# Kernel optimization log

Hardware: AMD Instinct MI355X
Metric: run time of the kernel (lower is better)

## Reference

```python
import jax, jax.numpy as jnp
import numpy as np

B, IN, H = 8192, 1024, 1024

def setup_inputs() -> dict:
    key = jax.random.key(0)
    ks = jax.random.split(key, 12)
    s_i = 1.0 / np.sqrt(IN)   # lecun-normal-ish scale for input kernels
    s_h = 1.0 / np.sqrt(H)
    d = {
        'inputs': jax.random.normal(ks[0], (B, IN), jnp.float32),
        'c': jax.random.normal(ks[1], (B, H), jnp.float32),
        'h': jax.random.normal(ks[2], (B, H), jnp.float32),
    }
    for n, k in zip(['Wii', 'Wif', 'Wig', 'Wio'], ks[3:7]):
        d[n] = jax.random.normal(k, (IN, H), jnp.float32) * s_i
    for n, k in zip(['Whi', 'Whf', 'Whg', 'Who'], ks[7:11]):
        d[n] = jax.random.normal(k, (H, H), jnp.float32) * s_h
    for n in ['bi', 'bf', 'bg', 'bo']:
        d[n] = jnp.zeros((H,), jnp.float32)
    return d

def reference(inputs, c, h, Wii, Wif, Wig, Wio, Whi, Whf, Whg, Who, bi, bf, bg, bo):
    # i = sigmoid(x Wii + h Whi + bi); f, o likewise; g = tanh(x Wig + h Whg + bg)
    i = jax.nn.sigmoid(inputs @ Wii + h @ Whi + bi)
    f = jax.nn.sigmoid(inputs @ Wif + h @ Whf + bf)
    g = jnp.tanh(inputs @ Wig + h @ Whg + bg)
    o = jax.nn.sigmoid(inputs @ Wio + h @ Who + bo)
    new_c = f * c + i * g
    new_h = o * jnp.tanh(new_c)
    return (new_c, new_h)
```

## Files before the change

kernel.cpp:

```cpp
#include <hip/hip_runtime.h>
#include <hip/hip_bf16.h>
#include <cstdint>


#define B_DIM 8192
#define H_DIM 1024
#define K2    2048
#define N4    4096
#define BK    64
#define BM    256
#define BN    256
#define NT    (K2 / BK)

typedef __bf16 bf16x8 __attribute__((ext_vector_type(8)));
typedef float  f32x4  __attribute__((ext_vector_type(4)));

__device__ __forceinline__ void async_load16(const __bf16* g, __bf16* l) {
  __builtin_amdgcn_global_load_lds(
      (__attribute__((address_space(1))) void*)(g),
      (__attribute__((address_space(3))) void*)(l),
      16, 0, 0);
}

__device__ __forceinline__ float sigm(float x) {
  return 1.0f / (1.0f + __expf(-x));
}
__device__ __forceinline__ float tanh_fast(float x) {
  return 2.0f / (1.0f + __expf(-2.0f * x)) - 1.0f;
}

__global__ void cast_a(const float* __restrict__ x, const float* __restrict__ h,
                       __bf16* __restrict__ A) {
  int row = blockIdx.x;
  int k = threadIdx.x << 3;
  const float* src = (k < H_DIM) ? (x + (size_t)row * H_DIM + k)
                                 : (h + (size_t)row * H_DIM + (k - H_DIM));
  float4 v0 = *(const float4*)src;
  float4 v1 = *(const float4*)(src + 4);
  bf16x8 o;
  o[0] = (__bf16)v0.x; o[1] = (__bf16)v0.y; o[2] = (__bf16)v0.z; o[3] = (__bf16)v0.w;
  o[4] = (__bf16)v1.x; o[5] = (__bf16)v1.y; o[6] = (__bf16)v1.z; o[7] = (__bf16)v1.w;
  *(bf16x8*)&A[(size_t)row * K2 + k] = o;
}

__global__ void cast_w(const float* __restrict__ Wii, const float* __restrict__ Wif,
                       const float* __restrict__ Wig, const float* __restrict__ Wio,
                       const float* __restrict__ Whi, const float* __restrict__ Whf,
                       const float* __restrict__ Whg, const float* __restrict__ Who,
                       __bf16* __restrict__ Bt) {
  __shared__ float tile[64][33];
  int k0 = blockIdx.x * 64;
  int j0 = blockIdx.y * 32;
  int gate = blockIdx.z;
  const float* Wi[4] = {Wii, Wif, Wig, Wio};
  const float* Wh[4] = {Whi, Whf, Whg, Who};
  const float* W = (k0 < H_DIM) ? Wi[gate] : Wh[gate];
  int kb = (k0 < H_DIM) ? k0 : (k0 - H_DIM);

  int col = threadIdx.x & 31;
  int rr  = threadIdx.x >> 5;
#pragma unroll
  for (int p = 0; p < 8; ++p)
    tile[p * 8 + rr][col] = W[(size_t)(kb + p * 8 + rr) * H_DIM + j0 + col];
  __syncthreads();

  int jj = threadIdx.x >> 3;
  int ko = threadIdx.x & 7;
  int j = j0 + jj;
  int p = ((j >> 4) << 6) + (gate << 4) + (j & 15);
  bf16x8 o;
#pragma unroll
  for (int t = 0; t < 8; ++t) o[t] = (__bf16)tile[ko * 8 + t][jj];
  *(bf16x8*)&Bt[(size_t)p * K2 + k0 + ko * 8] = o;
}


#define STAGE_A(D, KH, TT) do { \
    async_load16(gA0 + (size_t)(TT) * 64 + (KH) * 32, &As_s[D][KH][wave << 9]); \
    async_load16(gA1 + (size_t)(TT) * 64 + (KH) * 32, &As_s[D][KH][4096 + (wave << 9)]); \
  } while (0)
#define STAGE_B(D, KH, TT) do { \
    async_load16(gB0 + (size_t)(TT) * 64 + (KH) * 32, &Bs_s[D][KH][wave << 9]); \
    async_load16(gB1 + (size_t)(TT) * 64 + (KH) * 32, &Bs_s[D][KH][4096 + (wave << 9)]); \
  } while (0)

#define LOADA(D, KK, MH) do { \
    const __bf16* ap_ = &As_s[D][KK][(wm << 12) + ((MH) << 11) + lane_part]; \
    aF[0] = *(const bf16x8*)(ap_); \
    aF[1] = *(const bf16x8*)(ap_ + 512); \
    aF[2] = *(const bf16x8*)(ap_ + 1024); \
    aF[3] = *(const bf16x8*)(ap_ + 1536); \
  } while (0)
#define LOADB(D, KK) do { \
    const __bf16* bp_ = &Bs_s[D][KK][(wn << 11) + lane_part]; \
    bF[0] = *(const bf16x8*)(bp_); \
    bF[1] = *(const bf16x8*)(bp_ + 512); \
    bF[2] = *(const bf16x8*)(bp_ + 1024); \
    bF[3] = *(const bf16x8*)(bp_ + 1536); \
  } while (0)

#define BARW() do { \
    __builtin_amdgcn_s_barrier(); \
    asm volatile("s_waitcnt lgkmcnt(0)" ::: "memory"); \
    __builtin_amdgcn_sched_barrier(0); \
  } while (0)
#define ENDBAR() __builtin_amdgcn_s_barrier()
#define GATE8() asm volatile("s_waitcnt vmcnt(8)" ::: "memory")
#define GATE4() asm volatile("s_waitcnt vmcnt(4)" ::: "memory")
#define GATE0() asm volatile("s_waitcnt vmcnt(0)" ::: "memory")

#define MFMA_Q(MH) do { \
    __builtin_amdgcn_s_setprio(1); \
    _Pragma("unroll") \
    for (int i2 = 0; i2 < 4; ++i2) { \
      _Pragma("unroll") \
      for (int n2 = 0; n2 < 4; ++n2) \
        acc[(MH) * 4 + i2][n2] = __builtin_amdgcn_mfma_f32_16x16x32_bf16( \
            aF[i2], bF[n2], acc[(MH) * 4 + i2][n2], 0, 0, 0); \
    } \
    __builtin_amdgcn_s_setprio(0); \
  } while (0)

__global__ __launch_bounds__(512, 2) void lstm_gemm(
    const __bf16* __restrict__ A,
    const __bf16* __restrict__ Bt,
    const float* __restrict__ c,
    const float* __restrict__ bi, const float* __restrict__ bf_,
    const float* __restrict__ bg, const float* __restrict__ bo,
    float* __restrict__ out_c, float* __restrict__ out_h) {
  __shared__ __align__(16) __bf16 As_s[2][2][256 * 32];
  __shared__ __align__(16) __bf16 Bs_s[2][2][256 * 32];

  const int wg  = blockIdx.x;
  const int swz = ((wg & 7) << 6) + (wg >> 3);
  const int bx = swz & 31;
  const int by = swz >> 5;
  const int m0 = bx << 8;
  const int n0 = by << 8;

  const int tid  = threadIdx.x;
  const int wave = tid >> 6;
  const int lane = tid & 63;
  const int wm   = wave >> 2;
  const int wn   = wave & 3;

  const int srow = (wave << 4) + (lane >> 2);
  const int sgc  = (lane & 3) ^ ((lane >> 3) & 3);
  const __bf16* gA0 = A  + (size_t)(m0 + srow) * K2 + sgc * 8;
  const __bf16* gA1 = gA0 + (size_t)128 * K2;
  const __bf16* gB0 = Bt + (size_t)(n0 + srow) * K2 + sgc * 8;
  const __bf16* gB1 = gB0 + (size_t)128 * K2;

  const int lane_part = ((lane & 15) << 5) + ((((lane >> 4) ^ ((lane >> 1) & 3))) << 3);

  f32x4 acc[8][4] = {};
  bf16x8 aF[4], bF[4];

  STAGE_A(0, 0, 0); STAGE_B(0, 0, 0);
  STAGE_A(0, 1, 0); STAGE_B(0, 1, 0);
  STAGE_A(1, 0, 1); STAGE_B(1, 0, 1);
  GATE8();
  __builtin_amdgcn_s_barrier();

  for (int t = 0; t < NT - 2; ++t) {
    const int db = t & 1;
    LOADA(db, 0, 0); LOADB(db, 0); STAGE_A(db ^ 1, 1, t + 1);
    BARW(); MFMA_Q(0); ENDBAR();
    LOADA(db, 0, 1); STAGE_B(db ^ 1, 1, t + 1);
    BARW(); MFMA_Q(1); GATE8(); ENDBAR();
    LOADA(db, 1, 0); LOADB(db, 1); STAGE_A(db, 0, t + 2);
    BARW(); MFMA_Q(0); ENDBAR();
    LOADA(db, 1, 1); STAGE_B(db, 0, t + 2);
    BARW(); MFMA_Q(1); GATE8(); ENDBAR();
  }

  {
    LOADA(0, 0, 0); LOADB(0, 0); STAGE_A(1, 1, NT - 1);
    BARW(); MFMA_Q(0); ENDBAR();
    LOADA(0, 0, 1); STAGE_B(1, 1, NT - 1);
    BARW(); MFMA_Q(1); GATE8(); ENDBAR();
    LOADA(0, 1, 0); LOADB(0, 1);
    BARW(); MFMA_Q(0); ENDBAR();
    LOADA(0, 1, 1);
    BARW(); MFMA_Q(1); GATE4(); ENDBAR();
  }
  {
    LOADA(1, 0, 0); LOADB(1, 0);
    BARW(); MFMA_Q(0); ENDBAR();
    LOADA(1, 0, 1);
    BARW(); MFMA_Q(1); GATE0(); ENDBAR();
    LOADA(1, 1, 0); LOADB(1, 1);
    BARW(); MFMA_Q(0); ENDBAR();
    LOADA(1, 1, 1);
    BARW(); MFMA_Q(1);
  }

  const int jj = (by << 6) + (wn << 4) + (lane & 15);
  const float vbi = bi[jj], vbf = bf_[jj], vbg = bg[jj], vbo = bo[jj];
  const int row_base = m0 + (wm << 7) + ((lane >> 4) << 2);
#pragma unroll
  for (int mi = 0; mi < 8; ++mi) {
#pragma unroll
    for (int r = 0; r < 4; ++r) {
      const int row = row_base + mi * 16 + r;
      const size_t idx = (size_t)row * H_DIM + jj;
      const float gi = sigm(acc[mi][0][r] + vbi);
      const float gf = sigm(acc[mi][1][r] + vbf);
      const float gg = tanh_fast(acc[mi][2][r] + vbg);
      const float go = sigm(acc[mi][3][r] + vbo);
      const float cv = c[idx];
      const float nc = gf * cv + gi * gg;
      out_c[idx] = nc;
      out_h[idx] = go * tanh_fast(nc);
    }
  }
}

extern "C" void kernel_launch(void* const* d_in, const int* in_sizes, int n_in,
                              void* d_out, int out_size, void* d_ws, size_t ws_size,
                              hipStream_t stream) {
  const float* x   = (const float*)d_in[0];
  const float* c   = (const float*)d_in[1];
  const float* h   = (const float*)d_in[2];
  const float* Wii = (const float*)d_in[3];
  const float* Wif = (const float*)d_in[4];
  const float* Wig = (const float*)d_in[5];
  const float* Wio = (const float*)d_in[6];
  const float* Whi = (const float*)d_in[7];
  const float* Whf = (const float*)d_in[8];
  const float* Whg = (const float*)d_in[9];
  const float* Who = (const float*)d_in[10];
  const float* bi  = (const float*)d_in[11];
  const float* bf_ = (const float*)d_in[12];
  const float* bg  = (const float*)d_in[13];
  const float* bo  = (const float*)d_in[14];

  __bf16* Abf = (__bf16*)d_ws;
  __bf16* Bt  = (__bf16*)((char*)d_ws + (size_t)B_DIM * K2 * 2);

  float* out_c = (float*)d_out;
  float* out_h = out_c + (size_t)B_DIM * H_DIM;

  cast_a<<<B_DIM, 256, 0, stream>>>(x, h, Abf);
  dim3 gw(K2 / 64, H_DIM / 32, 4);
  cast_w<<<gw, 256, 0, stream>>>(Wii, Wif, Wig, Wio, Whi, Whf, Whg, Who, Bt);
  lstm_gemm<<<dim3((B_DIM / BM) * (N4 / BN)), 512, 0, stream>>>(
      Abf, Bt, c, bi, bf_, bg, bo, out_c, out_h);
}
```

Before: 360.8 us.

## Restructure GEMM main loop into 4 phases with one barrier each; widen cast kernels

The GEMM main loop goes from eight half-phases per two k-tiles, each with two barriers and an lgkmcnt wait, to four phases. Each phase loads all A and B fragments for a k-half, issues 32 MFMAs, and ends with one barrier. This cuts barrier and sync overhead and lets LDS reads overlap MFMAs, but holds more fragment registers live and drops the explicit lgkmcnt wait before the MFMAs. The cast kernels also do more work per block: 4 rows per block for the activation cast, and float4 loads over a 64x128 tile for the weight transpose.

New measurement: 335.4 us. 7.1% less time.

```diff
diff --git a/kernel.cpp b/kernel.cpp
--- a/kernel.cpp
+++ b/kernel.cpp
@@ -31,16 +31,22 @@
 
 __global__ void cast_a(const float* __restrict__ x, const float* __restrict__ h,
                        __bf16* __restrict__ A) {
-  int row = blockIdx.x;
-  int k = threadIdx.x << 3;
-  const float* src = (k < H_DIM) ? (x + (size_t)row * H_DIM + k)
-                                 : (h + (size_t)row * H_DIM + (k - H_DIM));
-  float4 v0 = *(const float4*)src;
-  float4 v1 = *(const float4*)(src + 4);
-  bf16x8 o;
-  o[0] = (__bf16)v0.x; o[1] = (__bf16)v0.y; o[2] = (__bf16)v0.z; o[3] = (__bf16)v0.w;
-  o[4] = (__bf16)v1.x; o[5] = (__bf16)v1.y; o[6] = (__bf16)v1.z; o[7] = (__bf16)v1.w;
-  *(bf16x8*)&A[(size_t)row * K2 + k] = o;
+  const int r0 = blockIdx.x << 2;
+  const int k = threadIdx.x << 3;
+  const float* base;
+  int koff;
+  if (k < H_DIM) { base = x; koff = k; } else { base = h; koff = k - H_DIM; }
+#pragma unroll
+  for (int r = 0; r < 4; ++r) {
+    const int row = r0 + r;
+    const float* src = base + (size_t)row * H_DIM + koff;
+    float4 v0 = *(const float4*)src;
+    float4 v1 = *(const float4*)(src + 4);
+    bf16x8 o;
+    o[0] = (__bf16)v0.x; o[1] = (__bf16)v0.y; o[2] = (__bf16)v0.z; o[3] = (__bf16)v0.w;
+    o[4] = (__bf16)v1.x; o[5] = (__bf16)v1.y; o[6] = (__bf16)v1.z; o[7] = (__bf16)v1.w;
+    *(bf16x8*)&A[(size_t)row * K2 + k] = o;
+  }
 }
 
 __global__ void cast_w(const float* __restrict__ Wii, const float* __restrict__ Wif,
@@ -48,30 +54,41 @@
                        const float* __restrict__ Whi, const float* __restrict__ Whf,
                        const float* __restrict__ Whg, const float* __restrict__ Who,
                        __bf16* __restrict__ Bt) {
-  __shared__ float tile[64][33];
-  int k0 = blockIdx.x * 64;
-  int j0 = blockIdx.y * 32;
-  int gate = blockIdx.z;
+  __shared__ float tile[64][132];
+  const int k0 = blockIdx.x * 64;
+  const int j0 = blockIdx.y * 128;
+  const int gate = blockIdx.z;
   const float* Wi[4] = {Wii, Wif, Wig, Wio};
   const float* Wh[4] = {Whi, Whf, Whg, Who};
   const float* W = (k0 < H_DIM) ? Wi[gate] : Wh[gate];
-  int kb = (k0 < H_DIM) ? k0 : (k0 - H_DIM);
-
-  int col = threadIdx.x & 31;
-  int rr  = threadIdx.x >> 5;
-#pragma unroll
-  for (int p = 0; p < 8; ++p)
-    tile[p * 8 + rr][col] = W[(size_t)(kb + p * 8 + rr) * H_DIM + j0 + col];
+  const int kb = (k0 < H_DIM) ? k0 : (k0 - H_DIM);
+
+  const int rr = threadIdx.x >> 3;
+  const int cs = threadIdx.x & 7;
+#pragma unroll
+  for (int pass = 0; pass < 2; ++pass) {
+    const int r = rr + pass * 32;
+    const float* src = W + (size_t)(kb + r) * H_DIM + j0;
+#pragma unroll
+    for (int i = 0; i < 4; ++i) {
+      float4 v = *(const float4*)(src + (cs + 8 * i) * 4);
+      *(float4*)&tile[r][(cs + 8 * i) * 4] = v;
+    }
+  }
   __syncthreads();
 
-  int jj = threadIdx.x >> 3;
-  int ko = threadIdx.x & 7;
-  int j = j0 + jj;
-  int p = ((j >> 4) << 6) + (gate << 4) + (j & 15);
-  bf16x8 o;
-#pragma unroll
-  for (int t = 0; t < 8; ++t) o[t] = (__bf16)tile[ko * 8 + t][jj];
-  *(bf16x8*)&Bt[(size_t)p * K2 + k0 + ko * 8] = o;
+  const int jl = threadIdx.x >> 1;
+  const int kc = (threadIdx.x & 1) * 32;
+  const int j  = j0 + jl;
+  const int p  = ((j >> 4) << 6) + (gate << 4) + (j & 15);
+  __bf16* dst = Bt + (size_t)p * K2 + k0 + kc;
+#pragma unroll
+  for (int cch = 0; cch < 4; ++cch) {
+    bf16x8 o;
+#pragma unroll
+    for (int e = 0; e < 8; ++e) o[e] = (__bf16)tile[kc + cch * 8 + e][jl];
+    *(bf16x8*)&dst[cch * 8] = o;
+  }
 }
 
 
@@ -83,42 +100,46 @@
     async_load16(gB0 + (size_t)(TT) * 64 + (KH) * 32, &Bs_s[D][KH][wave << 9]); \
     async_load16(gB1 + (size_t)(TT) * 64 + (KH) * 32, &Bs_s[D][KH][4096 + (wave << 9)]); \
   } while (0)
-
-#define LOADA(D, KK, MH) do { \
-    const __bf16* ap_ = &As_s[D][KK][(wm << 12) + ((MH) << 11) + lane_part]; \
-    aF[0] = *(const bf16x8*)(ap_); \
-    aF[1] = *(const bf16x8*)(ap_ + 512); \
-    aF[2] = *(const bf16x8*)(ap_ + 1024); \
-    aF[3] = *(const bf16x8*)(ap_ + 1536); \
-  } while (0)
-#define LOADB(D, KK) do { \
-    const __bf16* bp_ = &Bs_s[D][KK][(wn << 11) + lane_part]; \
-    bF[0] = *(const bf16x8*)(bp_); \
-    bF[1] = *(const bf16x8*)(bp_ + 512); \
-    bF[2] = *(const bf16x8*)(bp_ + 1024); \
-    bF[3] = *(const bf16x8*)(bp_ + 1536); \
-  } while (0)
-
-#define BARW() do { \
-    __builtin_amdgcn_s_barrier(); \
-    asm volatile("s_waitcnt lgkmcnt(0)" ::: "memory"); \
-    __builtin_amdgcn_sched_barrier(0); \
-  } while (0)
-#define ENDBAR() __builtin_amdgcn_s_barrier()
-#define GATE8() asm volatile("s_waitcnt vmcnt(8)" ::: "memory")
-#define GATE4() asm volatile("s_waitcnt vmcnt(4)" ::: "memory")
-#define GATE0() asm volatile("s_waitcnt vmcnt(0)" ::: "memory")
-
-#define MFMA_Q(MH) do { \
+#define STAGE_AB(D, KH, TT) do { STAGE_A(D, KH, TT); STAGE_B(D, KH, TT); } while (0)
+
+#define DS_LOADS(DB, KK) do { \
+    const __bf16* ap_ = &As_s[DB][KK][(wm << 12) + lane_part]; \
+    const __bf16* bp_ = &Bs_s[DB][KK][(wn << 11) + lane_part]; \
+    aF0[0] = *(const bf16x8*)(ap_);          aF0[1] = *(const bf16x8*)(ap_ + 512); \
+    aF0[2] = *(const bf16x8*)(ap_ + 1024);   aF0[3] = *(const bf16x8*)(ap_ + 1536); \
+    aF1[0] = *(const bf16x8*)(ap_ + 2048);   aF1[1] = *(const bf16x8*)(ap_ + 2560); \
+    aF1[2] = *(const bf16x8*)(ap_ + 3072);   aF1[3] = *(const bf16x8*)(ap_ + 3584); \
+    bF[0]  = *(const bf16x8*)(bp_);          bF[1]  = *(const bf16x8*)(bp_ + 512); \
+    bF[2]  = *(const bf16x8*)(bp_ + 1024);   bF[3]  = *(const bf16x8*)(bp_ + 1536); \
+  } while (0)
+
+#define MFMA32() do { \
     __builtin_amdgcn_s_setprio(1); \
     _Pragma("unroll") \
     for (int i2 = 0; i2 < 4; ++i2) { \
       _Pragma("unroll") \
       for (int n2 = 0; n2 < 4; ++n2) \
-        acc[(MH) * 4 + i2][n2] = __builtin_amdgcn_mfma_f32_16x16x32_bf16( \
-            aF[i2], bF[n2], acc[(MH) * 4 + i2][n2], 0, 0, 0); \
+        acc[i2][n2] = __builtin_amdgcn_mfma_f32_16x16x32_bf16( \
+            aF0[i2], bF[n2], acc[i2][n2], 0, 0, 0); \
+    } \
+    _Pragma("unroll") \
+    for (int i2 = 0; i2 < 4; ++i2) { \
+      _Pragma("unroll") \
+      for (int n2 = 0; n2 < 4; ++n2) \
+        acc[4 + i2][n2] = __builtin_amdgcn_mfma_f32_16x16x32_bf16( \
+            aF1[i2], bF[n2], acc[4 + i2][n2], 0, 0, 0); \
     } \
     __builtin_amdgcn_s_setprio(0); \
+  } while (0)
+
+#define GATE(N) asm volatile("s_waitcnt vmcnt(" #N ")" ::: "memory")
+
+#define PHASE(DB, KK, STG, GT) do { \
+    DS_LOADS(DB, KK); \
+    STG; \
+    MFMA32(); \
+    GT; \
+    __builtin_amdgcn_s_barrier(); \
   } while (0)
 
 __global__ __launch_bounds__(512, 2) void lstm_gemm(
@@ -154,46 +175,25 @@
   const int lane_part = ((lane & 15) << 5) + ((((lane >> 4) ^ ((lane >> 1) & 3))) << 3);
 
   f32x4 acc[8][4] = {};
-  bf16x8 aF[4], bF[4];
-
-  STAGE_A(0, 0, 0); STAGE_B(0, 0, 0);
-  STAGE_A(0, 1, 0); STAGE_B(0, 1, 0);
-  STAGE_A(1, 0, 1); STAGE_B(1, 0, 1);
-  GATE8();
+  bf16x8 aF0[4], aF1[4], bF[4];
+
+  STAGE_AB(0, 0, 0);
+  STAGE_AB(0, 1, 0);
+  STAGE_AB(1, 0, 1);
+  GATE(8);
   __builtin_amdgcn_s_barrier();
 
-  for (int t = 0; t < NT - 2; ++t) {
-    const int db = t & 1;
-    LOADA(db, 0, 0); LOADB(db, 0); STAGE_A(db ^ 1, 1, t + 1);
-    BARW(); MFMA_Q(0); ENDBAR();
-    LOADA(db, 0, 1); STAGE_B(db ^ 1, 1, t + 1);
-    BARW(); MFMA_Q(1); GATE8(); ENDBAR();
-    LOADA(db, 1, 0); LOADB(db, 1); STAGE_A(db, 0, t + 2);
-    BARW(); MFMA_Q(0); ENDBAR();
-    LOADA(db, 1, 1); STAGE_B(db, 0, t + 2);
-    BARW(); MFMA_Q(1); GATE8(); ENDBAR();
-  }
-
-  {
-    LOADA(0, 0, 0); LOADB(0, 0); STAGE_A(1, 1, NT - 1);
-    BARW(); MFMA_Q(0); ENDBAR();
-    LOADA(0, 0, 1); STAGE_B(1, 1, NT - 1);
-    BARW(); MFMA_Q(1); GATE8(); ENDBAR();
-    LOADA(0, 1, 0); LOADB(0, 1);
-    BARW(); MFMA_Q(0); ENDBAR();
-    LOADA(0, 1, 1);
-    BARW(); MFMA_Q(1); GATE4(); ENDBAR();
-  }
-  {
-    LOADA(1, 0, 0); LOADB(1, 0);
-    BARW(); MFMA_Q(0); ENDBAR();
-    LOADA(1, 0, 1);
-    BARW(); MFMA_Q(1); GATE0(); ENDBAR();
-    LOADA(1, 1, 0); LOADB(1, 1);
-    BARW(); MFMA_Q(0); ENDBAR();
-    LOADA(1, 1, 1);
-    BARW(); MFMA_Q(1);
-  }
+  for (int t = 0; t < NT - 2; t += 2) {
+    PHASE(0, 0, STAGE_AB(1, 1, t + 1), GATE(8));
+    PHASE(0, 1, STAGE_AB(0, 0, t + 2), GATE(8));
+    PHASE(1, 0, STAGE_AB(0, 1, t + 2), GATE(8));
+    PHASE(1, 1, STAGE_AB(1, 0, t + 3), GATE(8));
+  }
+  PHASE(0, 0, STAGE_AB(1, 1, NT - 1), GATE(8));
+  PHASE(0, 1, (void)0, GATE(4));
+  PHASE(1, 0, (void)0, GATE(0));
+  DS_LOADS(1, 1);
+  MFMA32();
 
   const int jj = (by << 6) + (wn << 4) + (lane & 15);
   const float vbi = bi[jj], vbf = bf_[jj], vbg = bg[jj], vbo = bo[jj];
@@ -241,8 +241,8 @@
   float* out_c = (float*)d_out;
   float* out_h = out_c + (size_t)B_DIM * H_DIM;
 
-  cast_a<<<B_DIM, 256, 0, stream>>>(x, h, Abf);
-  dim3 gw(K2 / 64, H_DIM / 32, 4);
+  cast_a<<<B_DIM / 4, 256, 0, stream>>>(x, h, Abf);
+  dim3 gw(K2 / 64, H_DIM / 128, 4);
   cast_w<<<gw, 256, 0, stream>>>(Wii, Wif, Wig, Wio, Whi, Whf, Whg, Who, Bt);
   lstm_gemm<<<dim3((B_DIM / BM) * (N4 / BN)), 512, 0, stream>>>(
       Abf, Bt, c, bi, bf_, bg, bo, out_c, out_h);
```

## Load B fragments directly from global in pre-swizzled layout, shrink tiles to 128x128

Applied to the files above, without the earlier changes.

Rewrites the weight pre-pack so B is stored in an MFMA-fragment-ready blocked layout, letting each wave read its B operands straight from global memory into registers instead of staging through LDS. The GEMM tile drops from 256x256 with 512 threads to 128x128 with 256 threads, only A is staged in a 4-deep LDS ring, and the grid swizzle is changed for XCD locality. This removes B's LDS traffic and several barriers per step and raises occupancy, at the cost of lower per-tile reuse, more total global/L2 reads of B and A, and exposed global latency on the B register loads.

Result: faster. 349.1 us (-3.2%).

```diff
diff --git a/kernel.cpp b/kernel.cpp
--- a/kernel.cpp
+++ b/kernel.cpp
@@ -7,10 +7,9 @@
 #define H_DIM 1024
 #define K2    2048
 #define N4    4096
-#define BK    64
-#define BM    256
-#define BN    256
-#define NT    (K2 / BK)
+#define BM    128
+#define BN    128
+#define NPH   64
 
 typedef __bf16 bf16x8 __attribute__((ext_vector_type(8)));
 typedef float  f32x4  __attribute__((ext_vector_type(4)));
@@ -64,145 +63,123 @@
     tile[p * 8 + rr][col] = W[(size_t)(kb + p * 8 + rr) * H_DIM + j0 + col];
   __syncthreads();
 
-  int jj = threadIdx.x >> 3;
-  int ko = threadIdx.x & 7;
-  int j = j0 + jj;
-  int p = ((j >> 4) << 6) + (gate << 4) + (j & 15);
+  const int jrow = threadIdx.x & 15;
+  const int seg  = (threadIdx.x >> 4) & 3;
+  const int kbl  = (threadIdx.x >> 6) & 1;
+  const int jh   = threadIdx.x >> 7;
+  const int j    = j0 + jh * 16 + jrow;
+  const int F    = ((j >> 4) << 2) + gate;
+  const int kblk = (k0 >> 5) + kbl;
   bf16x8 o;
 #pragma unroll
-  for (int t = 0; t < 8; ++t) o[t] = (__bf16)tile[ko * 8 + t][jj];
-  *(bf16x8*)&Bt[(size_t)p * K2 + k0 + ko * 8] = o;
-}
-
-
-#define STAGE_A(D, KH, TT) do { \
-    async_load16(gA0 + (size_t)(TT) * 64 + (KH) * 32, &As_s[D][KH][wave << 9]); \
-    async_load16(gA1 + (size_t)(TT) * 64 + (KH) * 32, &As_s[D][KH][4096 + (wave << 9)]); \
-  } while (0)
-#define STAGE_B(D, KH, TT) do { \
-    async_load16(gB0 + (size_t)(TT) * 64 + (KH) * 32, &Bs_s[D][KH][wave << 9]); \
-    async_load16(gB1 + (size_t)(TT) * 64 + (KH) * 32, &Bs_s[D][KH][4096 + (wave << 9)]); \
-  } while (0)
-
-#define LOADA(D, KK, MH) do { \
-    const __bf16* ap_ = &As_s[D][KK][(wm << 12) + ((MH) << 11) + lane_part]; \
+  for (int e = 0; e < 8; ++e) o[e] = (__bf16)tile[kbl * 32 + seg * 8 + e][jh * 16 + jrow];
+  *(bf16x8*)&Bt[((size_t)F * 64 + kblk) * 512 + (seg * 16 + jrow) * 8] = o;
+}
+
+
+#define BLOAD(DST, P1) do { \
+    DST[0] = *(const bf16x8*)(gB + (size_t)(P1) * 512); \
+    DST[1] = *(const bf16x8*)(gB + 32768 + (size_t)(P1) * 512); \
+    DST[2] = *(const bf16x8*)(gB + 65536 + (size_t)(P1) * 512); \
+    DST[3] = *(const bf16x8*)(gB + 98304 + (size_t)(P1) * 512); \
+  } while (0)
+
+#define ASTAGE(U, KB) do { \
+    async_load16(gA0 + (size_t)(KB) * 32, &As_s[U][wave << 9]); \
+    async_load16(gA1 + (size_t)(KB) * 32, &As_s[U][2048 + (wave << 9)]); \
+  } while (0)
+
+#define AREAD(U) do { \
+    const __bf16* ap_ = &As_s[U][a_off]; \
     aF[0] = *(const bf16x8*)(ap_); \
     aF[1] = *(const bf16x8*)(ap_ + 512); \
     aF[2] = *(const bf16x8*)(ap_ + 1024); \
     aF[3] = *(const bf16x8*)(ap_ + 1536); \
   } while (0)
-#define LOADB(D, KK) do { \
-    const __bf16* bp_ = &Bs_s[D][KK][(wn << 11) + lane_part]; \
-    bF[0] = *(const bf16x8*)(bp_); \
-    bF[1] = *(const bf16x8*)(bp_ + 512); \
-    bF[2] = *(const bf16x8*)(bp_ + 1024); \
-    bF[3] = *(const bf16x8*)(bp_ + 1536); \
-  } while (0)
-
-#define BARW() do { \
-    __builtin_amdgcn_s_barrier(); \
-    asm volatile("s_waitcnt lgkmcnt(0)" ::: "memory"); \
-    __builtin_amdgcn_sched_barrier(0); \
-  } while (0)
-#define ENDBAR() __builtin_amdgcn_s_barrier()
-#define GATE8() asm volatile("s_waitcnt vmcnt(8)" ::: "memory")
-#define GATE4() asm volatile("s_waitcnt vmcnt(4)" ::: "memory")
-#define GATE0() asm volatile("s_waitcnt vmcnt(0)" ::: "memory")
-
-#define MFMA_Q(MH) do { \
+
+#define MFMA16(BF) do { \
     __builtin_amdgcn_s_setprio(1); \
     _Pragma("unroll") \
-    for (int i2 = 0; i2 < 4; ++i2) { \
+    for (int mi = 0; mi < 4; ++mi) { \
       _Pragma("unroll") \
-      for (int n2 = 0; n2 < 4; ++n2) \
-        acc[(MH) * 4 + i2][n2] = __builtin_amdgcn_mfma_f32_16x16x32_bf16( \
-            aF[i2], bF[n2], acc[(MH) * 4 + i2][n2], 0, 0, 0); \
+      for (int tn = 0; tn < 4; ++tn) \
+        acc[mi][tn] = __builtin_amdgcn_mfma_f32_16x16x32_bf16( \
+            aF[mi], BF[tn], acc[mi][tn], 0, 0, 0); \
     } \
     __builtin_amdgcn_s_setprio(0); \
   } while (0)
 
-__global__ __launch_bounds__(512, 2) void lstm_gemm(
+#define GATE(N) asm volatile("s_waitcnt vmcnt(" #N ")" ::: "memory")
+#define BAR()   __builtin_amdgcn_s_barrier()
+
+#define PH(I, UST, BFU, BFL, P) do { \
+    AREAD(I); \
+    BLOAD(BFL, (P) + 1); \
+    MFMA16(BFU); \
+    ASTAGE(UST, (P) + 3); \
+    GATE(6); \
+    BAR(); \
+  } while (0)
+
+__global__ __launch_bounds__(256, 3) void lstm_gemm(
     const __bf16* __restrict__ A,
     const __bf16* __restrict__ Bt,
     const float* __restrict__ c,
     const float* __restrict__ bi, const float* __restrict__ bf_,
     const float* __restrict__ bg, const float* __restrict__ bo,
     float* __restrict__ out_c, float* __restrict__ out_h) {
-  __shared__ __align__(16) __bf16 As_s[2][2][256 * 32];
-  __shared__ __align__(16) __bf16 Bs_s[2][2][256 * 32];
+  __shared__ __align__(16) __bf16 As_s[4][128 * 32];
 
   const int wg  = blockIdx.x;
-  const int swz = ((wg & 7) << 6) + (wg >> 3);
-  const int bx = swz & 31;
-  const int by = swz >> 5;
-  const int m0 = bx << 8;
-  const int n0 = by << 8;
+  const int xcd = wg & 7;
+  const int ii  = wg >> 3;
+  const int bx  = (xcd << 3) + (ii & 7);
+  const int by  = ii >> 3;
+  const int m0  = bx << 7;
 
   const int tid  = threadIdx.x;
   const int wave = tid >> 6;
   const int lane = tid & 63;
-  const int wm   = wave >> 2;
-  const int wn   = wave & 3;
-
-  const int srow = (wave << 4) + (lane >> 2);
-  const int sgc  = (lane & 3) ^ ((lane >> 3) & 3);
-  const __bf16* gA0 = A  + (size_t)(m0 + srow) * K2 + sgc * 8;
-  const __bf16* gA1 = gA0 + (size_t)128 * K2;
-  const __bf16* gB0 = Bt + (size_t)(n0 + srow) * K2 + sgc * 8;
-  const __bf16* gB1 = gB0 + (size_t)128 * K2;
-
-  const int lane_part = ((lane & 15) << 5) + ((((lane >> 4) ^ ((lane >> 1) & 3))) << 3);
-
-  f32x4 acc[8][4] = {};
-  bf16x8 aF[4], bF[4];
-
-  STAGE_A(0, 0, 0); STAGE_B(0, 0, 0);
-  STAGE_A(0, 1, 0); STAGE_B(0, 1, 0);
-  STAGE_A(1, 0, 1); STAGE_B(1, 0, 1);
-  GATE8();
-  __builtin_amdgcn_s_barrier();
-
-  for (int t = 0; t < NT - 2; ++t) {
-    const int db = t & 1;
-    LOADA(db, 0, 0); LOADB(db, 0); STAGE_A(db ^ 1, 1, t + 1);
-    BARW(); MFMA_Q(0); ENDBAR();
-    LOADA(db, 0, 1); STAGE_B(db ^ 1, 1, t + 1);
-    BARW(); MFMA_Q(1); GATE8(); ENDBAR();
-    LOADA(db, 1, 0); LOADB(db, 1); STAGE_A(db, 0, t + 2);
-    BARW(); MFMA_Q(0); ENDBAR();
-    LOADA(db, 1, 1); STAGE_B(db, 0, t + 2);
-    BARW(); MFMA_Q(1); GATE8(); ENDBAR();
+  const int wm   = wave >> 1;
+  const int wn   = wave & 1;
+
+  const int srow = tid >> 2;
+  const int sgc  = (tid & 3) ^ ((tid >> 3) & 3);
+  const __bf16* gA0 = A + (size_t)(m0 + srow) * K2 + sgc * 8;
+  const __bf16* gA1 = gA0 + (size_t)64 * K2;
+
+  const __bf16* gB = Bt + (size_t)(by * 8 + wn * 4) * 32768 + lane * 8;
+
+  const int a_off = (wm << 11) + ((lane & 15) << 5) +
+                    (((lane >> 4) ^ ((lane >> 1) & 3)) << 3);
+
+  f32x4 acc[4][4] = {};
+  bf16x8 aF[4], bfa[4], bfb[4];
+
+  ASTAGE(0, 0); ASTAGE(1, 1); ASTAGE(2, 2);
+  BLOAD(bfa, 0);
+  GATE(8);
+  BAR();
+
+  for (int p0 = 0; p0 < 60; p0 += 4) {
+    PH(0, 3, bfa, bfb, p0 + 0);
+    PH(1, 0, bfb, bfa, p0 + 1);
+    PH(2, 1, bfa, bfb, p0 + 2);
+    PH(3, 2, bfb, bfa, p0 + 3);
   }
-
-  {
-    LOADA(0, 0, 0); LOADB(0, 0); STAGE_A(1, 1, NT - 1);
-    BARW(); MFMA_Q(0); ENDBAR();
-    LOADA(0, 0, 1); STAGE_B(1, 1, NT - 1);
-    BARW(); MFMA_Q(1); GATE8(); ENDBAR();
-    LOADA(0, 1, 0); LOADB(0, 1);
-    BARW(); MFMA_Q(0); ENDBAR();
-    LOADA(0, 1, 1);
-    BARW(); MFMA_Q(1); GATE4(); ENDBAR();
-  }
-  {
-    LOADA(1, 0, 0); LOADB(1, 0);
-    BARW(); MFMA_Q(0); ENDBAR();
-    LOADA(1, 0, 1);
-    BARW(); MFMA_Q(1); GATE0(); ENDBAR();
-    LOADA(1, 1, 0); LOADB(1, 1);
-    BARW(); MFMA_Q(0); ENDBAR();
-    LOADA(1, 1, 1);
-    BARW(); MFMA_Q(1);
-  }
-
-  const int jj = (by << 6) + (wn << 4) + (lane & 15);
+  AREAD(0); BLOAD(bfb, 61); MFMA16(bfa); ASTAGE(3, 63); GATE(6); BAR();
+  AREAD(1); BLOAD(bfa, 62); MFMA16(bfb); GATE(4); BAR();
+  AREAD(2); BLOAD(bfb, 63); MFMA16(bfa); GATE(0); BAR();
+  AREAD(3); MFMA16(bfb);
+
+  const int jj = (by << 5) + (wn << 4) + (lane & 15);
   const float vbi = bi[jj], vbf = bf_[jj], vbg = bg[jj], vbo = bo[jj];
-  const int row_base = m0 + (wm << 7) + ((lane >> 4) << 2);
-#pragma unroll
-  for (int mi = 0; mi < 8; ++mi) {
+  const int rb = m0 + (wm << 6) + ((lane >> 4) << 2);
+#pragma unroll
+  for (int mi = 0; mi < 4; ++mi) {
 #pragma unroll
     for (int r = 0; r < 4; ++r) {
-      const int row = row_base + mi * 16 + r;
+      const int row = rb + mi * 16 + r;
       const size_t idx = (size_t)row * H_DIM + jj;
       const float gi = sigm(acc[mi][0][r] + vbi);
       const float gf = sigm(acc[mi][1][r] + vbf);
@@ -244,6 +221,6 @@
   cast_a<<<B_DIM, 256, 0, stream>>>(x, h, Abf);
   dim3 gw(K2 / 64, H_DIM / 32, 4);
   cast_w<<<gw, 256, 0, stream>>>(Wii, Wif, Wig, Wio, Whi, Whf, Whg, Who, Bt);
-  lstm_gemm<<<dim3((B_DIM / BM) * (N4 / BN)), 512, 0, stream>>>(
+  lstm_gemm<<<dim3((B_DIM / BM) * (N4 / BN)), 256, 0, stream>>>(
       Abf, Bt, c, bi, bf_, bg, bo, out_c, out_h);
 }
```
